# Optimization experiments

Measured on AMD Instinct MI355X. Metric: run time of the kernel, lower is better.

Reference implementation:

```python
import jax, jax.numpy as jnp
import numpy as np
import math

DIM = 1024
NUM_HEADS = 16
HEAD_DIM = 64
SEQ_LEN = 2048
ATTN_SCALE = 0.12


def cosine_norm(x, eps=1e-12):
    # unit-normalize along last dim
    return x * jax.lax.rsqrt(jnp.sum(x * x, axis=-1, keepdims=True) + eps)


def rotary_tables(T, head_dim):
    dim_quarter = max(1, head_dim // 4)
    angular_freq = (1.0 / 1024.0) ** jnp.linspace(0.0, 1.0, dim_quarter, dtype=jnp.float32)
    angular_freq = jnp.concatenate([angular_freq, jnp.zeros(dim_quarter, dtype=jnp.float32)])  # [head_dim//2]
    t = jnp.arange(T, dtype=jnp.float32)
    theta = t[:, None] * angular_freq[None, :]  # [T, head_dim//2]
    return jnp.cos(theta), jnp.sin(theta)


def apply_rotary(x_BTHD, cos, sin):
    # cos/sin: [T, head_dim//2] -> broadcast [1, T, 1, head_dim//2]
    c = cos[None, :, None, :]
    s = sin[None, :, None, :]
    x1, x2 = jnp.split(x_BTHD, 2, axis=-1)
    y1 = x1 * c + x2 * s
    y2 = -x1 * s + x2 * c
    return jnp.concatenate([y1, y2], axis=-1)


def setup_inputs() -> dict:
    key = jax.random.key(0)
    ks = jax.random.split(key, 6)
    x = jax.random.normal(ks[0], (1, SEQ_LEN, DIM), dtype=jnp.float32)
    init_std = 0.02
    Wq = jax.random.normal(ks[1], (DIM, NUM_HEADS * HEAD_DIM), dtype=jnp.float32) * init_std
    Wk = jax.random.normal(ks[2], (DIM, NUM_HEADS * HEAD_DIM), dtype=jnp.float32) * init_std
    Wv = jax.random.normal(ks[3], (DIM, NUM_HEADS * HEAD_DIM), dtype=jnp.float32) * init_std
    Wo = jax.random.normal(ks[4], (NUM_HEADS * HEAD_DIM, DIM), dtype=jnp.float32) * init_std
    # Scale param: initialized as ones * (1/sqrt(dim)); use rand around that magnitude
    s_qk = jax.random.uniform(ks[5], (NUM_HEADS, HEAD_DIM), dtype=jnp.float32,
                              minval=0.5, maxval=1.5) * (1.0 / math.sqrt(DIM))
    return {"x": x, "Wq": Wq, "Wk": Wk, "Wv": Wv, "Wo": Wo, "s_qk": s_qk}


def reference(x, Wq, Wk, Wv, Wo, s_qk):
    B, T, _ = x.shape
    # projections
    q = (x @ Wq).reshape(B, T, NUM_HEADS, HEAD_DIM)
    k = (x @ Wk).reshape(B, T, NUM_HEADS, HEAD_DIM)
    v = (x @ Wv).reshape(B, T, NUM_HEADS, HEAD_DIM)
    # effective scale: s * (init/scale) with init=1, scale=1/sqrt(dim)
    s_eff = s_qk * math.sqrt(DIM)  # [H, D]
    q = cosine_norm(q) * s_eff[None, None, :, :]
    k = cosine_norm(k) * s_eff[None, None, :, :]
    cos, sin = rotary_tables(T, HEAD_DIM)
    q = apply_rotary(q, cos, sin)
    k = apply_rotary(k, cos, sin)
    # causal attention with fixed scale 0.12 (block_mask == causal)
    scores = jnp.einsum('bthd,bshd->bhts', q, k) * ATTN_SCALE  # [B,H,T,T]
    causal = jnp.tril(jnp.ones((T, T), dtype=bool))
    scores = jnp.where(causal[None, None, :, :], scores, jnp.float32(-1e30))
    attn = jax.nn.softmax(scores, axis=-1)
    y = jnp.einsum('bhts,bshd->bthd', attn, v)
    y = y.reshape(B, T, NUM_HEADS * HEAD_DIM)
    return y @ Wo
```

## Files before the change

kernel.cpp:

```cpp
#include <hip/hip_runtime.h>

typedef unsigned short u16;
typedef unsigned int u32;
typedef __attribute__((ext_vector_type(8))) short bf16x8;
typedef __attribute__((ext_vector_type(4))) float f32x4;

__device__ __forceinline__ u16 f2bf(float x) {
  unsigned u = __float_as_uint(x);
  u += 0x7fffu + ((u >> 16) & 1u);
  return (u16)(u >> 16);
}
__device__ __forceinline__ float bf2f(u16 z) {
  return __uint_as_float((u32)z << 16);
}
__device__ __forceinline__ u32 cvtpk(float lo, float hi) {
  u32 r;
  asm("v_cvt_pk_bf16_f32 %0, %1, %2" : "=v"(r) : "v"(lo), "v"(hi));
  return r;
}

__global__ __launch_bounds__(256) void prep(const float* __restrict__ x,
                                            const float* __restrict__ W0,
                                            const float* __restrict__ W1,
                                            const float* __restrict__ W2,
                                            const float* __restrict__ W3,
                                            u16* __restrict__ xb,
                                            u16* __restrict__ Wt,
                                            float2* __restrict__ rtab) {
  __shared__ alignas(16) u16 ls[64 * 72];
  int b = blockIdx.x;
  int tid = threadIdx.x;
  if (b < 2048) {
    int g = b * 256 + tid;
    int i = g * 4;
    float4 f = *(const float4*)(x + i);
    ushort4 o;
    o.x = f2bf(f.x); o.y = f2bf(f.y); o.z = f2bf(f.z); o.w = f2bf(f.w);
    *(ushort4*)(xb + i) = o;
    if (g < 2048 * 16) {
      int t = g >> 4, ii = g & 15;
      float fr = exp2f(-10.0f * (float)ii / 15.0f);
      float th = (float)t * fr;
      rtab[g] = make_float2(cosf(th), sinf(th));
    }
    return;
  }
  int bb = b - 2048;
  int z = bb >> 8;
  int rem = bb & 255;
  const float* W = (z == 0) ? W0 : (z == 1) ? W1 : (z == 2) ? W2 : W3;
  u16* o = Wt + (size_t)z * (1024u * 1024u);
  int kt = (rem >> 4) * 64, nt = (rem & 15) * 64;
  int r = tid >> 2, c0 = (tid & 3) * 16;
  const float* src = W + (size_t)(kt + r) * 1024 + nt + c0;
  u16 tmp[16];
#pragma unroll
  for (int c = 0; c < 16; c += 4) {
    float4 f = *(const float4*)(src + c);
    tmp[c + 0] = f2bf(f.x); tmp[c + 1] = f2bf(f.y);
    tmp[c + 2] = f2bf(f.z); tmp[c + 3] = f2bf(f.w);
  }
#pragma unroll
  for (int c = 0; c < 16; ++c) ls[r * 72 + c0 + c] = tmp[c];
  __syncthreads();
#pragma unroll
  for (int pass = 0; pass < 4; ++pass) {
    int n = pass * 16 + (tid >> 4);
    int kk = (tid & 15) * 4;
    ushort4 val;
    val.x = ls[(kk + 0) * 72 + n];
    val.y = ls[(kk + 1) * 72 + n];
    val.z = ls[(kk + 2) * 72 + n];
    val.w = ls[(kk + 3) * 72 + n];
    *(ushort4*)(o + (size_t)(nt + n) * 1024 + kt + kk) = val;
  }
}

#define GLD2 72

__global__ __launch_bounds__(512) void gemm_qkv(const u16* __restrict__ A,
                                                const u16* __restrict__ Wt,
                                                u16* __restrict__ qb,
                                                u16* __restrict__ kb,
                                                u16* __restrict__ vt,
                                                const float* __restrict__ s_qk,
                                                const float2* __restrict__ rtab) {
  __shared__ alignas(16) u16 As[128 * GLD2];
  __shared__ alignas(16) u16 Bs[128 * GLD2];
  int z = blockIdx.z;
  const u16* B = Wt + (size_t)z * (1024u * 1024u);
  int tid = threadIdx.x;
  int bm = blockIdx.y * 128, bn = blockIdx.x * 128;
  int lane = tid & 63, w = tid >> 6;
  int wm = (w >> 1) * 32, wn = (w & 1) * 64;
  int m16 = lane & 15, q = lane >> 4;
  f32x4 acc[2][4] = {};
  int srow = tid >> 2, scol = (tid & 3) * 16;
  const u16* aptr = A + (size_t)(bm + srow) * 1024 + scol;
  const u16* bptr = B + (size_t)(bn + srow) * 1024 + scol;
  uint4 a0 = *(const uint4*)(aptr);
  uint4 a1 = *(const uint4*)(aptr + 8);
  uint4 b0 = *(const uint4*)(bptr);
  uint4 b1 = *(const uint4*)(bptr + 8);
  for (int k0 = 0; k0 < 1024; k0 += 64) {
    __syncthreads();
    *(uint4*)&As[srow * GLD2 + scol] = a0;
    *(uint4*)&As[srow * GLD2 + scol + 8] = a1;
    *(uint4*)&Bs[srow * GLD2 + scol] = b0;
    *(uint4*)&Bs[srow * GLD2 + scol + 8] = b1;
    uint4 na0, na1, nb0, nb1;
    if (k0 < 960) {
      na0 = *(const uint4*)(aptr + k0 + 64);
      na1 = *(const uint4*)(aptr + k0 + 72);
      nb0 = *(const uint4*)(bptr + k0 + 64);
      nb1 = *(const uint4*)(bptr + k0 + 72);
    }
    __syncthreads();
#pragma unroll
    for (int kh = 0; kh < 2; ++kh) {
      bf16x8 af[2], bfr[4];
#pragma unroll
      for (int mt = 0; mt < 2; ++mt)
        af[mt] = *(const bf16x8*)&As[(wm + mt * 16 + m16) * GLD2 + kh * 32 + q * 8];
#pragma unroll
      for (int nt = 0; nt < 4; ++nt)
        bfr[nt] = *(const bf16x8*)&Bs[(wn + nt * 16 + m16) * GLD2 + kh * 32 + q * 8];
#pragma unroll
      for (int mt = 0; mt < 2; ++mt)
#pragma unroll
        for (int nt = 0; nt < 4; ++nt)
          acc[mt][nt] = __builtin_amdgcn_mfma_f32_16x16x32_bf16(af[mt], bfr[nt], acc[mt][nt], 0, 0, 0);
    }
    if (k0 < 960) { a0 = na0; a1 = na1; b0 = nb0; b1 = nb1; }
  }
  int hh = (bn + wn) >> 6;
  if (z == 2) {
#pragma unroll
    for (int nt = 0; nt < 4; ++nt) {
      int n = bn + wn + nt * 16 + m16;
#pragma unroll
      for (int mt = 0; mt < 2; ++mt) {
        int t0 = bm + wm + mt * 16 + q * 4;
        ushort4 val;
        val.x = f2bf(acc[mt][nt][0]);
        val.y = f2bf(acc[mt][nt][1]);
        val.z = f2bf(acc[mt][nt][2]);
        val.w = f2bf(acc[mt][nt][3]);
        *(ushort4*)(vt + (size_t)n * 2048 + t0) = val;
      }
    }
  } else {
    u16* dst = z ? kb : qb;
    float se0 = s_qk[hh * 64 +  0 + m16] * 32.0f;
    float se1 = s_qk[hh * 64 + 16 + m16] * 32.0f;
    float se2 = s_qk[hh * 64 + 32 + m16] * 32.0f;
    float se3 = s_qk[hh * 64 + 48 + m16] * 32.0f;
#pragma unroll
    for (int mt = 0; mt < 2; ++mt)
#pragma unroll
      for (int r = 0; r < 4; ++r) {
        float ss = acc[mt][0][r] * acc[mt][0][r] + acc[mt][1][r] * acc[mt][1][r]
                 + acc[mt][2][r] * acc[mt][2][r] + acc[mt][3][r] * acc[mt][3][r];
        ss += __shfl_xor(ss, 1); ss += __shfl_xor(ss, 2);
        ss += __shfl_xor(ss, 4); ss += __shfl_xor(ss, 8);
        float inv = rsqrtf(ss + 1e-12f);
        int t = bm + wm + mt * 16 + q * 4 + r;
        float2 cs = rtab[t * 16 + m16];
        float x0 = acc[mt][0][r] * inv * se0;
        float x1 = acc[mt][1][r] * inv * se1;
        float x2 = acc[mt][2][r] * inv * se2;
        float x3 = acc[mt][3][r] * inv * se3;
        size_t off = (size_t)t * 1024 + hh * 64 + m16;
        dst[off]      = f2bf(x0 * cs.x + x2 * cs.y);
        dst[off + 16] = f2bf(x1);
        dst[off + 32] = f2bf(x2 * cs.x - x0 * cs.y);
        dst[off + 48] = f2bf(x3);
      }
  }
}

#define PLD 40
#define RPD 20
__global__ __launch_bounds__(256) void attn_flash(const u16* __restrict__ qb,
                                                  const u16* __restrict__ kb,
                                                  const u16* __restrict__ vt,
                                                  u16* __restrict__ yb) {
  __shared__ alignas(16) unsigned char smb[12 * 64 * RPD * 4 + 4 * 64 * 4];
  int h = blockIdx.x;
  int y = blockIdx.y;
  int qt = (y < 16) ? (31 - y) : (y - 16);
  int t0 = qt * 64;
  int tid = threadIdx.x;
  int lane = tid & 63, w = tid >> 6;
  int m16 = lane & 15, q = lane >> 4;
  u16* pw = (u16*)smb + w * 64 * PLD;
  bf16x8 qa[4][2];
#pragma unroll
  for (int qn = 0; qn < 4; ++qn) {
    const u16* qr = qb + (size_t)(t0 + qn * 16 + m16) * 1024 + h * 64;
    qa[qn][0] = *(const bf16x8*)(qr + q * 8);
    qa[qn][1] = *(const bf16x8*)(qr + 32 + q * 8);
  }
  int wk = w * 32;
  const u16* kbase = kb + (size_t)(wk + m16) * 1024 + h * 64 + q * 8;
  const u16* vbase = vt + (size_t)(h * 64 + m16) * 2048 + wk + q * 8;
  f32x4 Yacc[4][4] = {};
  float lsum[4] = {0.f, 0.f, 0.f, 0.f};
  int nkb = (qt + 2) >> 1;
  bf16x8 kfr[2][2], vfr[4];
#pragma unroll
  for (int kt = 0; kt < 2; ++kt) {
    kfr[kt][0] = *(const bf16x8*)(kbase + kt * 16384);
    kfr[kt][1] = *(const bf16x8*)(kbase + kt * 16384 + 32);
  }
#pragma unroll
  for (int nt = 0; nt < 4; ++nt)
    vfr[nt] = *(const bf16x8*)(vbase + (size_t)nt * 32768);
  for (int kbi = 0; kbi < nkb; ++kbi) {
    int kb0 = kbi * 128;
    f32x4 ST[2][4] = {};
    __builtin_amdgcn_s_setprio(1);
#pragma unroll
    for (int kt = 0; kt < 2; ++kt)
#pragma unroll
      for (int qn = 0; qn < 4; ++qn) {
        ST[kt][qn] = __builtin_amdgcn_mfma_f32_16x16x32_bf16(kfr[kt][0], qa[qn][0], ST[kt][qn], 0, 0, 0);
        ST[kt][qn] = __builtin_amdgcn_mfma_f32_16x16x32_bf16(kfr[kt][1], qa[qn][1], ST[kt][qn], 0, 0, 0);
      }
    __builtin_amdgcn_s_setprio(0);
    bf16x8 kn[2][2], vn[4];
    bool more = (kbi + 1 < nkb);
    if (more) {
      const u16* kp = kbase + (size_t)(kb0 + 128) * 1024;
#pragma unroll
      for (int kt = 0; kt < 2; ++kt) {
        kn[kt][0] = *(const bf16x8*)(kp + kt * 16384);
        kn[kt][1] = *(const bf16x8*)(kp + kt * 16384 + 32);
      }
#pragma unroll
      for (int nt = 0; nt < 4; ++nt)
        vn[nt] = *(const bf16x8*)(vbase + (size_t)nt * 32768 + kb0 + 128);
    }
    bool last = (kbi == nkb - 1);
#pragma unroll
    for (int kt = 0; kt < 2; ++kt) {
      int keyb = kb0 + wk + kt * 16 + q * 4;
#pragma unroll
      for (int qn = 0; qn < 4; ++qn) {
        int qr_ = t0 + qn * 16 + m16;
        float p0 = __builtin_amdgcn_exp2f(ST[kt][qn][0] * 0.17312340490667562f);
        float p1 = __builtin_amdgcn_exp2f(ST[kt][qn][1] * 0.17312340490667562f);
        float p2 = __builtin_amdgcn_exp2f(ST[kt][qn][2] * 0.17312340490667562f);
        float p3 = __builtin_amdgcn_exp2f(ST[kt][qn][3] * 0.17312340490667562f);
        if (last) {
          p0 = (keyb + 0 <= qr_) ? p0 : 0.f;
          p1 = (keyb + 1 <= qr_) ? p1 : 0.f;
          p2 = (keyb + 2 <= qr_) ? p2 : 0.f;
          p3 = (keyb + 3 <= qr_) ? p3 : 0.f;
        }
        lsum[qn] += (p0 + p1) + (p2 + p3);
        uint2 pk2;
        pk2.x = cvtpk(p0, p1);
        pk2.y = cvtpk(p2, p3);
        *(uint2*)&pw[(qn * 16 + m16) * PLD + kt * 16 + q * 4] = pk2;
      }
    }
    bf16x8 pa[4];
#pragma unroll
    for (int qn = 0; qn < 4; ++qn)
      pa[qn] = *(const bf16x8*)&pw[(qn * 16 + m16) * PLD + q * 8];
    __builtin_amdgcn_s_setprio(1);
#pragma unroll
    for (int qn = 0; qn < 4; ++qn)
#pragma unroll
      for (int nt = 0; nt < 4; ++nt)
        Yacc[qn][nt] = __builtin_amdgcn_mfma_f32_16x16x32_bf16(pa[qn], vfr[nt], Yacc[qn][nt], 0, 0, 0);
    __builtin_amdgcn_s_setprio(0);
    if (more) {
      kfr[0][0] = kn[0][0]; kfr[0][1] = kn[0][1];
      kfr[1][0] = kn[1][0]; kfr[1][1] = kn[1][1];
      vfr[0] = vn[0]; vfr[1] = vn[1]; vfr[2] = vn[2]; vfr[3] = vn[3];
    }
  }
#pragma unroll
  for (int qn = 0; qn < 4; ++qn) {
    lsum[qn] += __shfl_xor(lsum[qn], 16);
    lsum[qn] += __shfl_xor(lsum[qn], 32);
  }
  __syncthreads();
  float* Yr = (float*)smb;
  float* Lb = (float*)(smb + 12 * 64 * RPD * 4);
  if (q == 0) {
#pragma unroll
    for (int qn = 0; qn < 4; ++qn) Lb[w * 64 + qn * 16 + m16] = lsum[qn];
  }
#pragma unroll
  for (int qn = 0; qn < 4; ++qn) {
    if (qn != w) {
      int idx = w * 3 + (qn < w ? qn : qn - 1);
      float* dst = Yr + idx * 64 * RPD;
#pragma unroll
      for (int nt = 0; nt < 4; ++nt)
        *(f32x4*)&dst[(nt * 16 + m16) * RPD + q * 4] = Yacc[qn][nt];
    }
  }
  __syncthreads();
  float Lt[4];
#pragma unroll
  for (int r = 0; r < 4; ++r) {
    int row = w * 16 + q * 4 + r;
    Lt[r] = ((Lb[row] + Lb[64 + row]) + (Lb[128 + row] + Lb[192 + row]));
  }
#pragma unroll
  for (int nt = 0; nt < 4; ++nt) {
    f32x4 y2 = {0.f, 0.f, 0.f, 0.f};
#pragma unroll
    for (int qn = 0; qn < 4; ++qn)
      if (qn == w) y2 = Yacc[qn][nt];
#pragma unroll
    for (int wp = 0; wp < 4; ++wp) {
      if (wp != w) {
        int idx = wp * 3 + (w < wp ? w : w - 1);
        f32x4 o = *(const f32x4*)&Yr[idx * 64 * RPD + (nt * 16 + m16) * RPD + q * 4];
        y2 += o;
      }
    }
#pragma unroll
    for (int r = 0; r < 4; ++r) {
      int t = t0 + w * 16 + q * 4 + r;
      yb[(size_t)t * 1024 + h * 64 + nt * 16 + m16] =
          f2bf(y2[r] * __builtin_amdgcn_rcpf(Lt[r]));
    }
  }
}

__global__ __launch_bounds__(512) void gemm_o(const u16* __restrict__ A,
                                              const u16* __restrict__ B,
                                              float* __restrict__ C) {
  __shared__ alignas(16) u16 As[128 * GLD2];
  __shared__ alignas(16) u16 Bs[64 * GLD2];
  int tid = threadIdx.x;
  int bm = blockIdx.y * 128, bn = blockIdx.x * 64;
  int lane = tid & 63, w = tid >> 6;
  int wm = (w >> 1) * 32, wn = (w & 1) * 32;
  int m16 = lane & 15, q = lane >> 4;
  f32x4 acc[2][2] = {};
  int srA = tid >> 2, scA = (tid & 3) * 16;
  int srB = tid >> 3, scB = (tid & 7) * 8;
  const u16* aptr = A + (size_t)(bm + srA) * 1024 + scA;
  const u16* bptr = B + (size_t)(bn + srB) * 1024 + scB;
  uint4 a0 = *(const uint4*)(aptr);
  uint4 a1 = *(const uint4*)(aptr + 8);
  uint4 b0 = *(const uint4*)(bptr);
  for (int k0 = 0; k0 < 1024; k0 += 64) {
    __syncthreads();
    *(uint4*)&As[srA * GLD2 + scA] = a0;
    *(uint4*)&As[srA * GLD2 + scA + 8] = a1;
    *(uint4*)&Bs[srB * GLD2 + scB] = b0;
    uint4 na0, na1, nb0;
    if (k0 < 960) {
      na0 = *(const uint4*)(aptr + k0 + 64);
      na1 = *(const uint4*)(aptr + k0 + 72);
      nb0 = *(const uint4*)(bptr + k0 + 64);
    }
    __syncthreads();
#pragma unroll
    for (int kh = 0; kh < 2; ++kh) {
      bf16x8 af[2], bfr[2];
#pragma unroll
      for (int mt = 0; mt < 2; ++mt)
        af[mt] = *(const bf16x8*)&As[(wm + mt * 16 + m16) * GLD2 + kh * 32 + q * 8];
#pragma unroll
      for (int nt = 0; nt < 2; ++nt)
        bfr[nt] = *(const bf16x8*)&Bs[(wn + nt * 16 + m16) * GLD2 + kh * 32 + q * 8];
#pragma unroll
      for (int mt = 0; mt < 2; ++mt)
#pragma unroll
        for (int nt = 0; nt < 2; ++nt)
          acc[mt][nt] = __builtin_amdgcn_mfma_f32_16x16x32_bf16(af[mt], bfr[nt], acc[mt][nt], 0, 0, 0);
    }
    if (k0 < 960) { a0 = na0; a1 = na1; b0 = nb0; }
  }
#pragma unroll
  for (int mt = 0; mt < 2; ++mt)
#pragma unroll
    for (int nt = 0; nt < 2; ++nt)
#pragma unroll
      for (int r = 0; r < 4; ++r) {
        int row = bm + wm + mt * 16 + q * 4 + r;
        int col = bn + wn + nt * 16 + m16;
        C[(size_t)row * 1024 + col] = acc[mt][nt][r];
      }
}

extern "C" void kernel_launch(void* const* d_in, const int* in_sizes, int n_in,
                              void* d_out, int out_size, void* d_ws, size_t ws_size,
                              hipStream_t stream) {
  const float* x   = (const float*)d_in[0];
  const float* Wq  = (const float*)d_in[1];
  const float* Wk  = (const float*)d_in[2];
  const float* Wv  = (const float*)d_in[3];
  const float* Wo  = (const float*)d_in[4];
  const float* sqk = (const float*)d_in[5];
  float* out = (float*)d_out;
  char* ws = (char*)d_ws;

  u16*    xb   = (u16*)ws;
  u16*    Wt   = (u16*)(ws + ((size_t)4 << 20));
  float2* rtab = (float2*)(ws + ((size_t)12 << 20));
  u16*    qb16 = (u16*)(ws + ((size_t)16 << 20));
  u16*    kb16 = (u16*)(ws + ((size_t)20 << 20));
  u16*    vt16 = (u16*)(ws + ((size_t)24 << 20));
  u16*    yb   = (u16*)(ws + ((size_t)28 << 20));
  u16*    Wto  = Wt + (size_t)3 * 1024 * 1024;

  prep<<<3072, 256, 0, stream>>>(x, Wq, Wk, Wv, Wo, xb, Wt, rtab);
  gemm_qkv<<<dim3(8, 16, 3), 512, 0, stream>>>(xb, Wt, qb16, kb16, vt16, sqk, rtab);
  attn_flash<<<dim3(16, 32), 256, 0, stream>>>(qb16, kb16, vt16, yb);
  gemm_o<<<dim3(16, 16), 512, 0, stream>>>(yb, Wto, out);
}
```

Before: 136.8 us.

## Fuse x bf16 conversion into QKV GEMM and software-pipeline PV matmul in attention

```diff
diff --git a/kernel.cpp b/kernel.cpp
--- a/kernel.cpp
+++ b/kernel.cpp
@@ -19,35 +19,24 @@
   return r;
 }
 
-__global__ __launch_bounds__(256) void prep(const float* __restrict__ x,
-                                            const float* __restrict__ W0,
+__global__ __launch_bounds__(256) void prep(const float* __restrict__ W0,
                                             const float* __restrict__ W1,
                                             const float* __restrict__ W2,
                                             const float* __restrict__ W3,
-                                            u16* __restrict__ xb,
                                             u16* __restrict__ Wt,
                                             float2* __restrict__ rtab) {
   __shared__ alignas(16) u16 ls[64 * 72];
   int b = blockIdx.x;
   int tid = threadIdx.x;
-  if (b < 2048) {
+  if (b < 128) {
     int g = b * 256 + tid;
-    int i = g * 4;
-    float4 f = *(const float4*)(x + i);
-    ushort4 o;
-    o.x = f2bf(f.x); o.y = f2bf(f.y); o.z = f2bf(f.z); o.w = f2bf(f.w);
-    *(ushort4*)(xb + i) = o;
-    if (g < 2048 * 16) {
-      int t = g >> 4, ii = g & 15;
-      float fr = exp2f(-10.0f * (float)ii / 15.0f);
-      float th = (float)t * fr;
-      rtab[g] = make_float2(cosf(th), sinf(th));
-    }
-    return;
-  }
-  int bb = b - 2048;
-  int z = bb >> 8;
-  int rem = bb & 255;
+    int t = g >> 4, ii = g & 15;
+    float fr = exp2f(-10.0f * (float)ii / 15.0f);
+    float th = (float)t * fr;
+    rtab[g] = make_float2(cosf(th), sinf(th));
+  }
+  int z = b >> 8;
+  int rem = b & 255;
   const float* W = (z == 0) ? W0 : (z == 1) ? W1 : (z == 2) ? W2 : W3;
   u16* o = Wt + (size_t)z * (1024u * 1024u);
   int kt = (rem >> 4) * 64, nt = (rem & 15) * 64;
@@ -78,7 +67,7 @@
 
 #define GLD2 72
 
-__global__ __launch_bounds__(512) void gemm_qkv(const u16* __restrict__ A,
+__global__ __launch_bounds__(512) void gemm_qkv(const float* __restrict__ X,
                                                 const u16* __restrict__ Wt,
                                                 u16* __restrict__ qb,
                                                 u16* __restrict__ kb,
@@ -96,22 +85,31 @@
   int m16 = lane & 15, q = lane >> 4;
   f32x4 acc[2][4] = {};
   int srow = tid >> 2, scol = (tid & 3) * 16;
-  const u16* aptr = A + (size_t)(bm + srow) * 1024 + scol;
+  const float* ax = X + (size_t)(bm + srow) * 1024 + scol;
   const u16* bptr = B + (size_t)(bn + srow) * 1024 + scol;
-  uint4 a0 = *(const uint4*)(aptr);
-  uint4 a1 = *(const uint4*)(aptr + 8);
+  float4 fa0 = *(const float4*)(ax);
+  float4 fa1 = *(const float4*)(ax + 4);
+  float4 fa2 = *(const float4*)(ax + 8);
+  float4 fa3 = *(const float4*)(ax + 12);
   uint4 b0 = *(const uint4*)(bptr);
   uint4 b1 = *(const uint4*)(bptr + 8);
   for (int k0 = 0; k0 < 1024; k0 += 64) {
     __syncthreads();
-    *(uint4*)&As[srow * GLD2 + scol] = a0;
-    *(uint4*)&As[srow * GLD2 + scol + 8] = a1;
+    uint4 pk0, pk1;
+    pk0.x = cvtpk(fa0.x, fa0.y); pk0.y = cvtpk(fa0.z, fa0.w);
+    pk0.z = cvtpk(fa1.x, fa1.y); pk0.w = cvtpk(fa1.z, fa1.w);
+    pk1.x = cvtpk(fa2.x, fa2.y); pk1.y = cvtpk(fa2.z, fa2.w);
+    pk1.z = cvtpk(fa3.x, fa3.y); pk1.w = cvtpk(fa3.z, fa3.w);
+    *(uint4*)&As[srow * GLD2 + scol] = pk0;
+    *(uint4*)&As[srow * GLD2 + scol + 8] = pk1;
     *(uint4*)&Bs[srow * GLD2 + scol] = b0;
     *(uint4*)&Bs[srow * GLD2 + scol + 8] = b1;
-    uint4 na0, na1, nb0, nb1;
+    uint4 nb0, nb1;
     if (k0 < 960) {
-      na0 = *(const uint4*)(aptr + k0 + 64);
-      na1 = *(const uint4*)(aptr + k0 + 72);
+      fa0 = *(const float4*)(ax + k0 + 64);
+      fa1 = *(const float4*)(ax + k0 + 68);
+      fa2 = *(const float4*)(ax + k0 + 72);
+      fa3 = *(const float4*)(ax + k0 + 76);
       nb0 = *(const uint4*)(bptr + k0 + 64);
       nb1 = *(const uint4*)(bptr + k0 + 72);
     }
@@ -131,7 +129,7 @@
         for (int nt = 0; nt < 4; ++nt)
           acc[mt][nt] = __builtin_amdgcn_mfma_f32_16x16x32_bf16(af[mt], bfr[nt], acc[mt][nt], 0, 0, 0);
     }
-    if (k0 < 960) { a0 = na0; a1 = na1; b0 = nb0; b1 = nb1; }
+    if (k0 < 960) { b0 = nb0; b1 = nb1; }
   }
   int hh = (bn + wn) >> 6;
   if (z == 2) {
@@ -193,7 +191,8 @@
   int tid = threadIdx.x;
   int lane = tid & 63, w = tid >> 6;
   int m16 = lane & 15, q = lane >> 4;
-  u16* pw = (u16*)smb + w * 64 * PLD;
+  u16* pw0 = (u16*)smb + w * 64 * PLD;
+  u16* pw1 = (u16*)smb + (4 + w) * 64 * PLD;
   bf16x8 qa[4][2];
 #pragma unroll
   for (int qn = 0; qn < 4; ++qn) {
@@ -207,15 +206,13 @@
   f32x4 Yacc[4][4] = {};
   float lsum[4] = {0.f, 0.f, 0.f, 0.f};
   int nkb = (qt + 2) >> 1;
-  bf16x8 kfr[2][2], vfr[4];
+  bf16x8 kfr[2][2];
+  bf16x8 vfr[4] = {};
 #pragma unroll
   for (int kt = 0; kt < 2; ++kt) {
     kfr[kt][0] = *(const bf16x8*)(kbase + kt * 16384);
     kfr[kt][1] = *(const bf16x8*)(kbase + kt * 16384 + 32);
   }
-#pragma unroll
-  for (int nt = 0; nt < 4; ++nt)
-    vfr[nt] = *(const bf16x8*)(vbase + (size_t)nt * 32768);
   for (int kbi = 0; kbi < nkb; ++kbi) {
     int kb0 = kbi * 128;
     f32x4 ST[2][4] = {};
@@ -228,7 +225,11 @@
         ST[kt][qn] = __builtin_amdgcn_mfma_f32_16x16x32_bf16(kfr[kt][1], qa[qn][1], ST[kt][qn], 0, 0, 0);
       }
     __builtin_amdgcn_s_setprio(0);
-    bf16x8 kn[2][2], vn[4];
+    bf16x8 vn[4];
+#pragma unroll
+    for (int nt = 0; nt < 4; ++nt)
+      vn[nt] = *(const bf16x8*)(vbase + (size_t)nt * 32768 + kb0);
+    bf16x8 kn[2][2];
     bool more = (kbi + 1 < nkb);
     if (more) {
       const u16* kp = kbase + (size_t)(kb0 + 128) * 1024;
@@ -237,10 +238,13 @@
         kn[kt][0] = *(const bf16x8*)(kp + kt * 16384);
         kn[kt][1] = *(const bf16x8*)(kp + kt * 16384 + 32);
       }
-#pragma unroll
-      for (int nt = 0; nt < 4; ++nt)
-        vn[nt] = *(const bf16x8*)(vbase + (size_t)nt * 32768 + kb0 + 128);
-    }
+    }
+    u16* pwp = (kbi & 1) ? pw0 : pw1;
+    u16* pwc = (kbi & 1) ? pw1 : pw0;
+    bf16x8 pa[4];
+#pragma unroll
+    for (int qn = 0; qn < 4; ++qn)
+      pa[qn] = *(const bf16x8*)&pwp[(qn * 16 + m16) * PLD + q * 8];
     bool last = (kbi == nkb - 1);
 #pragma unroll
     for (int kt = 0; kt < 2; ++kt) {
@@ -262,25 +266,37 @@
         uint2 pk2;
         pk2.x = cvtpk(p0, p1);
         pk2.y = cvtpk(p2, p3);
-        *(uint2*)&pw[(qn * 16 + m16) * PLD + kt * 16 + q * 4] = pk2;
-      }
-    }
-    bf16x8 pa[4];
-#pragma unroll
-    for (int qn = 0; qn < 4; ++qn)
-      pa[qn] = *(const bf16x8*)&pw[(qn * 16 + m16) * PLD + q * 8];
-    __builtin_amdgcn_s_setprio(1);
-#pragma unroll
-    for (int qn = 0; qn < 4; ++qn)
-#pragma unroll
-      for (int nt = 0; nt < 4; ++nt)
-        Yacc[qn][nt] = __builtin_amdgcn_mfma_f32_16x16x32_bf16(pa[qn], vfr[nt], Yacc[qn][nt], 0, 0, 0);
-    __builtin_amdgcn_s_setprio(0);
+        *(uint2*)&pwc[(qn * 16 + m16) * PLD + kt * 16 + q * 4] = pk2;
+      }
+    }
+    if (kbi) {
+      __builtin_amdgcn_s_setprio(1);
+#pragma unroll
+      for (int qn = 0; qn < 4; ++qn)
+#pragma unroll
+        for (int nt = 0; nt < 4; ++nt)
+          Yacc[qn][nt] = __builtin_amdgcn_mfma_f32_16x16x32_bf16(pa[qn], vfr[nt], Yacc[qn][nt], 0, 0, 0);
+      __builtin_amdgcn_s_setprio(0);
+    }
+    vfr[0] = vn[0]; vfr[1] = vn[1]; vfr[2] = vn[2]; vfr[3] = vn[3];
     if (more) {
       kfr[0][0] = kn[0][0]; kfr[0][1] = kn[0][1];
       kfr[1][0] = kn[1][0]; kfr[1][1] = kn[1][1];
-      vfr[0] = vn[0]; vfr[1] = vn[1]; vfr[2] = vn[2]; vfr[3] = vn[3];
-    }
+    }
+  }
+  {
+    u16* pwl = ((nkb - 1) & 1) ? pw1 : pw0;
+    bf16x8 pl[4];
+#pragma unroll
+    for (int qn = 0; qn < 4; ++qn)
+      pl[qn] = *(const bf16x8*)&pwl[(qn * 16 + m16) * PLD + q * 8];
+    __builtin_amdgcn_s_setprio(1);
+#pragma unroll
+    for (int qn = 0; qn < 4; ++qn)
+#pragma unroll
+      for (int nt = 0; nt < 4; ++nt)
+        Yacc[qn][nt] = __builtin_amdgcn_mfma_f32_16x16x32_bf16(pl[qn], vfr[nt], Yacc[qn][nt], 0, 0, 0);
+    __builtin_amdgcn_s_setprio(0);
   }
 #pragma unroll
   for (int qn = 0; qn < 4; ++qn) {
@@ -405,7 +421,6 @@
   float* out = (float*)d_out;
   char* ws = (char*)d_ws;
 
-  u16*    xb   = (u16*)ws;
   u16*    Wt   = (u16*)(ws + ((size_t)4 << 20));
   float2* rtab = (float2*)(ws + ((size_t)12 << 20));
   u16*    qb16 = (u16*)(ws + ((size_t)16 << 20));
@@ -414,8 +429,8 @@
   u16*    yb   = (u16*)(ws + ((size_t)28 << 20));
   u16*    Wto  = Wt + (size_t)3 * 1024 * 1024;
 
-  prep<<<3072, 256, 0, stream>>>(x, Wq, Wk, Wv, Wo, xb, Wt, rtab);
-  gemm_qkv<<<dim3(8, 16, 3), 512, 0, stream>>>(xb, Wt, qb16, kb16, vt16, sqk, rtab);
+  prep<<<1024, 256, 0, stream>>>(Wq, Wk, Wv, Wo, Wt, rtab);
+  gemm_qkv<<<dim3(8, 16, 3), 512, 0, stream>>>(x, Wt, qb16, kb16, vt16, sqk, rtab);
   attn_flash<<<dim3(16, 32), 256, 0, stream>>>(qb16, kb16, vt16, yb);
   gemm_o<<<dim3(16, 16), 512, 0, stream>>>(yb, Wto, out);
 }
```

Result: slower. 139.7 us (+2.1%).
